# Performance work log

Measured on AMD Instinct MI355X. Metric: run time of the kernel, lower is better.

Reference implementation:

```python
import jax, jax.numpy as jnp
import numpy as np

N = 4096
D_IN = 512
D_H = 128
HEADS = 4
NEG_BIG = 1e10  # matches tf mask constant
LEAKY_ALPHA = 0.2  # tf.nn.leaky_relu default


def setup_inputs() -> dict:
    key = jax.random.key(0)
    ks = jax.random.split(key, 6)
    # 0/1 dense adjacency (faithful to tf.sparse.add producing dense 0/1 + mask)
    adjacency = jax.random.randint(ks[0], (N, N), 0, 2).astype(jnp.float32)
    # guarantee no empty rows (softmax over all -1e10 is degenerate)
    adjacency = adjacency.at[jnp.arange(N), jnp.arange(N)].set(1.0)
    input_feature = jax.random.normal(ks[1], (N, D_IN), dtype=jnp.float32)
    scale = 1.0 / np.sqrt(D_IN)
    kernels = jax.random.normal(ks[2], (HEADS, D_IN, D_H), dtype=jnp.float32) * scale
    biases = jnp.zeros((HEADS, D_H), dtype=jnp.float32)
    a_scale = 1.0 / np.sqrt(D_H)
    attn_self = jax.random.normal(ks[3], (HEADS, D_H), dtype=jnp.float32) * a_scale
    attn_neigh = jax.random.normal(ks[4], (HEADS, D_H), dtype=jnp.float32) * a_scale
    return {
        "adjacency": adjacency,
        "input_feature": input_feature,
        "kernels": kernels,
        "biases": biases,
        "attn_self": attn_self,
        "attn_neigh": attn_neigh,
    }


def reference(adjacency, input_feature, kernels, biases, attn_self, attn_neigh):
    # per-head feature projection: [H, N, D_h]
    feats = jnp.einsum("nd,hde->hne", input_feature, kernels)
    # additive attention logits
    a_s = jnp.einsum("hne,he->hn", feats, attn_self)   # [H, N]
    a_n = jnp.einsum("hne,he->hn", feats, attn_neigh)  # [H, N]
    dense = a_s[:, :, None] + a_n[:, None, :]          # [H, N, N]
    dense = jax.nn.leaky_relu(dense, negative_slope=LEAKY_ALPHA)
    mask = NEG_BIG * (adjacency - 1.0)                 # 0 where edge, -1e10 elsewhere
    dense = jax.nn.softmax(dense + mask[None, :, :], axis=-1)
    out = jnp.einsum("hnm,hme->hne", dense, feats) + biases[:, None, :]  # [H, N, D_h]
    # concat heads: [N, H*D_h]
    return jnp.transpose(out, (1, 0, 2)).reshape(out.shape[1], -1)
```

## Files before the change

### kernel.cpp

```cpp
#include <hip/hip_runtime.h>

#define NN 4096
#define DIN 512
#define DH 128
#define NH 4

typedef float f32x4 __attribute__((ext_vector_type(4)));
typedef _Float16 f16x8 __attribute__((ext_vector_type(8)));
typedef _Float16 f16x4 __attribute__((ext_vector_type(4)));

__device__ __forceinline__ float leaky(float x){ return x > 0.f ? x : 0.2f*x; }

__global__ __launch_bounds__(256) void k_pack(
    const float* __restrict__ adj, unsigned int* __restrict__ bmg)
{
  int tId = blockIdx.x*256 + threadIdx.x;
  const float* p = adj + (size_t)tId*32;
  unsigned int b = 0;
  #pragma unroll
  for (int k=0;k<8;k++){
    f32x4 v = *(const f32x4*)(p + k*4);
    #pragma unroll
    for (int q=0;q<4;q++) b |= (v[q] > 0.5f) ? (1u << (k*4+q)) : 0u;
  }
  bmg[tId] = b;
}

__global__ __launch_bounds__(256) void k_gemm1(
    const float* __restrict__ X, const float* __restrict__ Kw,
    const float* __restrict__ attn_s, const float* __restrict__ attn_n,
    _Float16* __restrict__ featsT, float* __restrict__ a_s, float* __restrict__ a_n)
{
  const int it = blockIdx.x, h = blockIdx.y;
  const int i0 = it*64;
  const int t = threadIdx.x, w = t>>6, lane = t&63;
  const int eoff = (w>>1)*64, ioff = (w&1)*32;
  const int lg = lane>>4, li = lane&15;

  __shared__ _Float16 KT[128][40];
  __shared__ _Float16 XT[64][40];
  __shared__ float red_s[2][2][2][16];
  __shared__ float red_n[2][2][2][16];

  f32x4 acc[4][2] = {};

  for (int ks=0; ks<16; ++ks){
    const int d0 = ks*32;
    __syncthreads();
    #pragma unroll
    for (int q=0;q<4;q++){
      int f = t + 256*q;
      int e = f & 127, dg = (f>>7)*4;
      f16x4 hv;
      #pragma unroll
      for (int k=0;k<4;k++)
        hv[k] = (_Float16)Kw[(h*DIN + d0 + dg + k)*DH + e];
      *(f16x4*)&KT[e][dg] = hv;
    }
    #pragma unroll
    for (int q=0;q<2;q++){
      int f = t + 256*q;
      int i = f>>3, s = (f&7)*4;
      f32x4 v = *(const f32x4*)&X[(i0+i)*DIN + d0 + s];
      f16x4 hv; hv[0]=(_Float16)v[0]; hv[1]=(_Float16)v[1];
      hv[2]=(_Float16)v[2]; hv[3]=(_Float16)v[3];
      *(f16x4*)&XT[i][s] = hv;
    }
    __syncthreads();
    f16x8 af[4], bf[2];
    #pragma unroll
    for (int ef=0; ef<4; ++ef) af[ef] = *(const f16x8*)&KT[eoff + ef*16 + li][lg*8];
    #pragma unroll
    for (int f2=0; f2<2; ++f2) bf[f2] = *(const f16x8*)&XT[ioff + f2*16 + li][lg*8];
    #pragma unroll
    for (int ef=0; ef<4; ++ef)
      #pragma unroll
      for (int f2=0; f2<2; ++f2)
        acc[ef][f2] = __builtin_amdgcn_mfma_f32_16x16x32_f16(af[ef], bf[f2], acc[ef][f2], 0,0,0);
  }

  float ps[2] = {0,0}, pn[2] = {0,0};
  #pragma unroll
  for (int ef=0; ef<4; ++ef){
    #pragma unroll
    for (int r=0;r<4;r++){
      int e = eoff + ef*16 + lg*4 + r;
      float as_e = attn_s[h*DH + e];
      float an_e = attn_n[h*DH + e];
      #pragma unroll
      for (int f2=0; f2<2; ++f2){
        int irow = i0 + ioff + f2*16 + li;
        float v = acc[ef][f2][r];
        featsT[(h*DH + e)*NN + irow] = (_Float16)v;
        ps[f2] += v*as_e; pn[f2] += v*an_e;
      }
    }
  }
  #pragma unroll
  for (int f2=0; f2<2; ++f2){
    ps[f2] += __shfl_xor(ps[f2], 16); ps[f2] += __shfl_xor(ps[f2], 32);
    pn[f2] += __shfl_xor(pn[f2], 16); pn[f2] += __shfl_xor(pn[f2], 32);
  }
  if (lane < 16){
    red_s[w>>1][w&1][0][lane] = ps[0]; red_s[w>>1][w&1][1][lane] = ps[1];
    red_n[w>>1][w&1][0][lane] = pn[0]; red_n[w>>1][w&1][1][lane] = pn[1];
  }
  __syncthreads();
  if (t < 64){
    int ih = t>>5, fb = (t>>4)&1, l2 = t&15;
    a_s[h*NN + i0 + t] = red_s[0][ih][fb][l2] + red_s[1][ih][fb][l2];
    a_n[h*NN + i0 + t] = red_n[0][ih][fb][l2] + red_n[1][ih][fb][l2];
  }
}

__global__ void k_amax(const float* __restrict__ a_n, float* __restrict__ Amax){
  int h = blockIdx.x, t = threadIdx.x;
  float m = -3.4e38f;
  for (int i=t; i<NN; i+=256) m = fmaxf(m, a_n[h*NN+i]);
  #pragma unroll
  for (int s=1; s<64; s<<=1) m = fmaxf(m, __shfl_xor(m, s));
  __shared__ float sm[4];
  if ((t&63)==0) sm[t>>6] = m;
  __syncthreads();
  if (t==0) Amax[h] = fmaxf(fmaxf(sm[0],sm[1]), fmaxf(sm[2],sm[3]));
}

__global__ __launch_bounds__(512, 4) void k_pv(
    const unsigned int* __restrict__ bmg, const _Float16* __restrict__ featsT,
    const float* __restrict__ a_s, const float* __restrict__ a_n,
    const float* __restrict__ Amax,
    _Float16* __restrict__ Opart, float* __restrict__ Dpart)
{
  const int it = blockIdx.x, h = blockIdx.y, jcI = blockIdx.z;
  const int i0 = it*128, j0 = jcI*1024;
  const int t = threadIdx.x, w = t>>6, lane = t&63;
  const int lg = lane>>4, li = lane&15;

  __shared__ _Float16 ft[128*32];
  __shared__ float an_s[1024];
  __shared__ unsigned char bm_s[128*144];

  if (t < 256) *(f32x4*)&an_s[t*4] = *(const f32x4*)&a_n[h*NN + j0 + t*4];
  #pragma unroll
  for (int p=0;p<2;p++){
    int rr = p*64 + (t>>3), c = t&7;
    uint4 v = *(const uint4*)((const char*)bmg + (size_t)(i0+rr)*(NN/8) + jcI*128 + c*16);
    *(uint4*)&bm_s[rr*144 + c*16] = v;
  }
  const int rowA = i0 + w*16 + li;
  const float asv = a_s[h*NN + rowA];
  const float mv = leaky(asv + Amax[h]);
  const float negmc = -mv * 1.44269504f;
  __syncthreads();

  f32x4 acc[8] = {};
  f32x4 accd = {};
  f16x8 ones;
  #pragma unroll
  for (int q=0;q<8;q++) ones[q] = (_Float16)1.0f;

  const int e_st = t>>2, c_st = t&3;
  const size_t src_row = (size_t)(h*DH + e_st)*NN + j0 + c_st*8;

  for (int js=0; js<32; ++js){
    __syncthreads();
    __builtin_amdgcn_global_load_lds(
        (const __attribute__((address_space(1))) void*)(featsT + src_row + js*32),
        (__attribute__((address_space(3))) void*)(&ft[t*8]),
        16, 0, 0);

    const int jb = js*32 + lg*8;
    f32x4 an0 = *(const f32x4*)&an_s[jb];
    f32x4 an1 = *(const f32x4*)&an_s[jb+4];
    unsigned int byte = bm_s[(w*16+li)*144 + js*4 + lg];
    f16x8 af;
    #pragma unroll
    for (int q=0;q<8;q++){
      float anv = (q<4) ? an0[q] : an1[q-4];
      float x = asv + anv;
      float l = fmaxf(x, 0.2f*x);
      float e2 = __builtin_exp2f(fmaf(l, 1.44269504f, negmc));
      float wv = (byte & (1u<<q)) ? e2 : 0.f;
      af[q] = (_Float16)wv;
    }
    __syncthreads();
    #pragma unroll
    for (int ef=0; ef<8; ++ef){
      f16x8 bfr = *(const f16x8*)&ft[(ef*16+li)*32 + lg*8];
      acc[ef] = __builtin_amdgcn_mfma_f32_16x16x32_f16(af, bfr, acc[ef], 0,0,0);
    }
    accd = __builtin_amdgcn_mfma_f32_16x16x32_f16(af, ones, accd, 0,0,0);
  }

  const size_t chb = (size_t)(jcI*4 + h)*NN;
  if (li == 0)
    *(f32x4*)&Dpart[chb + i0 + w*16 + lg*4] = accd;
  #pragma unroll
  for (int ef=0; ef<8; ++ef)
    #pragma unroll
    for (int r=0;r<4;r++){
      int row = i0 + w*16 + lg*4 + r;
      Opart[(chb + row)*DH + ef*16 + li] = (_Float16)acc[ef][r];
    }
}

__global__ __launch_bounds__(256) void k_out(
    const _Float16* __restrict__ Opart, const float* __restrict__ Dpart,
    const float* __restrict__ bias, float* __restrict__ out)
{
  int gid = blockIdx.x*256 + threadIdx.x;
  int base = gid*4;
  int i = base >> 9;
  int he = base & 511;
  int h = he >> 7;
  int e = he & 127;
  float n0=0,n1=0,n2=0,n3=0, den=0;
  #pragma unroll
  for (int jc=0; jc<4; ++jc){
    int ch = (jc*4+h)*NN + i;
    f16x4 v = *(const f16x4*)(Opart + (size_t)ch*DH + e);
    n0 += (float)v[0]; n1 += (float)v[1]; n2 += (float)v[2]; n3 += (float)v[3];
    den += Dpart[ch];
  }
  float inv = 1.f/den;
  f32x4 b4 = *(const f32x4*)&bias[he];
  f32x4 o; o[0]=n0*inv+b4[0]; o[1]=n1*inv+b4[1]; o[2]=n2*inv+b4[2]; o[3]=n3*inv+b4[3];
  *(f32x4*)&out[base] = o;
}

extern "C" void kernel_launch(void* const* d_in, const int* in_sizes, int n_in,
                              void* d_out, int out_size, void* d_ws, size_t ws_size,
                              hipStream_t stream)
{
  const float* adj   = (const float*)d_in[0];
  const float* X     = (const float*)d_in[1];
  const float* Kw    = (const float*)d_in[2];
  const float* bias  = (const float*)d_in[3];
  const float* atn_s = (const float*)d_in[4];
  const float* atn_n = (const float*)d_in[5];
  float* out = (float*)d_out;

  char* ws = (char*)d_ws;
  _Float16* featsT = (_Float16*)ws;
  unsigned int* bmg = (unsigned int*)(ws + ((size_t)4<<20));
  float* a_s  = (float*)(ws + (size_t)6*1024*1024);
  float* a_n  = a_s + NH*NN;
  float* Amax = a_n + NH*NN;
  float* Dpart = Amax + 64;
  _Float16* Opart = (_Float16*)(Dpart + 4*NH*NN);

  hipLaunchKernelGGL(k_pack, dim3(2048), dim3(256), 0, stream, adj, bmg);
  hipLaunchKernelGGL(k_gemm1, dim3(64,4), dim3(256), 0, stream,
                     X, Kw, atn_s, atn_n, featsT, a_s, a_n);
  hipLaunchKernelGGL(k_amax, dim3(4), dim3(256), 0, stream, a_n, Amax);
  hipLaunchKernelGGL(k_pv, dim3(32,4,4), dim3(512), 0, stream,
                     bmg, featsT, a_s, a_n, Amax, Opart, Dpart);
  hipLaunchKernelGGL(k_out, dim3(2048), dim3(256), 0, stream,
                     Opart, Dpart, bias, out);
}
```

Before: 85.36 us.

## Factor exp of leaky logits into per-row and per-column terms, double-buffer features

Uses the identity exp(leaky(as+an)-m) = max(E_i*ea_j, G_i*ga_j), with exp(an) and exp(0.2*an) computed once per column in the amax kernel, so the per-element exp in the attention-weight loop becomes two multiplies and a max. The PV kernel moves to 256 threads with each wave handling two 16-row tiles that share each B-fragment load. Feature tiles are double-buffered with async global-to-LDS loads and an XOR-swizzled layout, leaving one barrier per iteration. The trade-offs are more registers for the doubled accumulators, possible overflow or underflow of exp(an) in fp32, and extra global buffers for the precomputed exponentials.

```diff
diff --git a/kernel.cpp b/kernel.cpp
--- a/kernel.cpp
+++ b/kernel.cpp
@@ -4,6 +4,7 @@
 #define DIN 512
 #define DH 128
 #define NH 4
+#define L2E 1.44269504f
 
 typedef float f32x4 __attribute__((ext_vector_type(4)));
 typedef _Float16 f16x8 __attribute__((ext_vector_type(8)));
@@ -113,10 +114,16 @@
   }
 }
 
-__global__ void k_amax(const float* __restrict__ a_n, float* __restrict__ Amax){
+__global__ void k_amax(const float* __restrict__ a_n, float* __restrict__ Amax,
+                       float* __restrict__ EA_g, float* __restrict__ GA_g){
   int h = blockIdx.x, t = threadIdx.x;
   float m = -3.4e38f;
-  for (int i=t; i<NN; i+=256) m = fmaxf(m, a_n[h*NN+i]);
+  for (int i=t; i<NN; i+=256){
+    float v = a_n[h*NN+i];
+    m = fmaxf(m, v);
+    EA_g[h*NN+i] = __builtin_exp2f(v*L2E);
+    GA_g[h*NN+i] = __builtin_exp2f(0.2f*v*L2E);
+  }
   #pragma unroll
   for (int s=1; s<64; s<<=1) m = fmaxf(m, __shfl_xor(m, s));
   __shared__ float sm[4];
@@ -125,10 +132,10 @@
   if (t==0) Amax[h] = fmaxf(fmaxf(sm[0],sm[1]), fmaxf(sm[2],sm[3]));
 }
 
-__global__ __launch_bounds__(512, 4) void k_pv(
+__global__ __launch_bounds__(256, 3) void k_pv(
     const unsigned int* __restrict__ bmg, const _Float16* __restrict__ featsT,
-    const float* __restrict__ a_s, const float* __restrict__ a_n,
-    const float* __restrict__ Amax,
+    const float* __restrict__ a_s, const float* __restrict__ Amax,
+    const float* __restrict__ EA_g, const float* __restrict__ GA_g,
     _Float16* __restrict__ Opart, float* __restrict__ Dpart)
 {
   const int it = blockIdx.x, h = blockIdx.y, jcI = blockIdx.z;
@@ -136,71 +143,108 @@
   const int t = threadIdx.x, w = t>>6, lane = t&63;
   const int lg = lane>>4, li = lane&15;
 
-  __shared__ _Float16 ft[128*32];
-  __shared__ float an_s[1024];
+  __shared__ _Float16 ft[2][128*32];
+  __shared__ float EA_s[1024], GA_s[1024];
   __shared__ unsigned char bm_s[128*144];
 
-  if (t < 256) *(f32x4*)&an_s[t*4] = *(const f32x4*)&a_n[h*NN + j0 + t*4];
-  #pragma unroll
-  for (int p=0;p<2;p++){
-    int rr = p*64 + (t>>3), c = t&7;
-    uint4 v = *(const uint4*)((const char*)bmg + (size_t)(i0+rr)*(NN/8) + jcI*128 + c*16);
-    *(uint4*)&bm_s[rr*144 + c*16] = v;
-  }
-  const int rowA = i0 + w*16 + li;
-  const float asv = a_s[h*NN + rowA];
-  const float mv = leaky(asv + Amax[h]);
-  const float negmc = -mv * 1.44269504f;
+  __builtin_amdgcn_global_load_lds(
+      (const __attribute__((address_space(1))) void*)(EA_g + h*NN + j0 + t*4),
+      (__attribute__((address_space(3))) void*)(&EA_s[t*4]), 16, 0, 0);
+  __builtin_amdgcn_global_load_lds(
+      (const __attribute__((address_space(1))) void*)(GA_g + h*NN + j0 + t*4),
+      (__attribute__((address_space(3))) void*)(&GA_s[t*4]), 16, 0, 0);
+  #pragma unroll
+  for (int p=0;p<4;p++){
+    int idx = p*256 + t;
+    int r = idx>>3, c = idx&7;
+    uint4 v = *(const uint4*)((const char*)bmg + (size_t)(i0+r)*(NN/8) + jcI*128 + c*16);
+    *(uint4*)&bm_s[r*144 + c*16] = v;
+  }
+
+  const int r0 = w*32 + li, r1 = r0 + 16;
+  const float am = Amax[h];
+  const float as0 = a_s[h*NN + i0 + r0];
+  const float as1 = a_s[h*NN + i0 + r1];
+  const float m0 = leaky(as0 + am), m1 = leaky(as1 + am);
+  const float E0 = __builtin_exp2f((as0 - m0)*L2E);
+  const float G0 = __builtin_exp2f((0.2f*as0 - m0)*L2E);
+  const float E1 = __builtin_exp2f((as1 - m1)*L2E);
+  const float G1 = __builtin_exp2f((0.2f*as1 - m1)*L2E);
+
+  auto STAGE = [&](int buf, int js){
+    #pragma unroll
+    for (int q=0;q<2;q++){
+      int idx = q*256 + t;
+      int r = idx>>2, p = idx&3;
+      int l = p ^ ((r>>1)&3);
+      __builtin_amdgcn_global_load_lds(
+          (const __attribute__((address_space(1))) void*)(featsT + (size_t)(h*DH + r)*NN + j0 + js*32 + l*8),
+          (__attribute__((address_space(3))) void*)(&ft[buf][idx*8]), 16, 0, 0);
+    }
+  };
+
+  STAGE(0, 0);
   __syncthreads();
 
-  f32x4 acc[8] = {};
-  f32x4 accd = {};
+  f32x4 acc0[8] = {}, acc1[8] = {};
+  f32x4 accd0 = {}, accd1 = {};
   f16x8 ones;
   #pragma unroll
   for (int q=0;q<8;q++) ones[q] = (_Float16)1.0f;
 
-  const int e_st = t>>2, c_st = t&3;
-  const size_t src_row = (size_t)(h*DH + e_st)*NN + j0 + c_st*8;
+  const int slot = lg ^ ((li>>1)&3);
 
   for (int js=0; js<32; ++js){
+    const int cur = js&1;
+    if (js < 31) STAGE(cur^1, js+1);
+
+    const int jb = js*32 + lg*8;
+    f32x4 ea0 = *(const f32x4*)&EA_s[jb];
+    f32x4 ea1 = *(const f32x4*)&EA_s[jb+4];
+    f32x4 ga0 = *(const f32x4*)&GA_s[jb];
+    f32x4 ga1 = *(const f32x4*)&GA_s[jb+4];
+    unsigned int b0 = bm_s[r0*144 + js*4 + lg];
+    unsigned int b1 = bm_s[r1*144 + js*4 + lg];
+
+    f16x8 af0, af1;
+    #pragma unroll
+    for (int q=0;q<8;q++){
+      float ev = (q<4) ? ea0[q] : ea1[q-4];
+      float gv = (q<4) ? ga0[q] : ga1[q-4];
+      float w0 = fmaxf(E0*ev, G0*gv);
+      float w1 = fmaxf(E1*ev, G1*gv);
+      unsigned mq0 = (unsigned)(((int)(b0 << (31-q))) >> 31);
+      unsigned mq1 = (unsigned)(((int)(b1 << (31-q))) >> 31);
+      w0 = __builtin_bit_cast(float, __builtin_bit_cast(unsigned, w0) & mq0);
+      w1 = __builtin_bit_cast(float, __builtin_bit_cast(unsigned, w1) & mq1);
+      af0[q] = (_Float16)w0;
+      af1[q] = (_Float16)w1;
+    }
+
+    #pragma unroll
+    for (int ef=0; ef<8; ++ef){
+      f16x8 bfr = *(const f16x8*)&ft[cur][(ef*16+li)*32 + slot*8];
+      acc0[ef] = __builtin_amdgcn_mfma_f32_16x16x32_f16(af0, bfr, acc0[ef], 0,0,0);
+      acc1[ef] = __builtin_amdgcn_mfma_f32_16x16x32_f16(af1, bfr, acc1[ef], 0,0,0);
+    }
+    accd0 = __builtin_amdgcn_mfma_f32_16x16x32_f16(af0, ones, accd0, 0,0,0);
+    accd1 = __builtin_amdgcn_mfma_f32_16x16x32_f16(af1, ones, accd1, 0,0,0);
+
     __syncthreads();
-    __builtin_amdgcn_global_load_lds(
-        (const __attribute__((address_space(1))) void*)(featsT + src_row + js*32),
-        (__attribute__((address_space(3))) void*)(&ft[t*8]),
-        16, 0, 0);
-
-    const int jb = js*32 + lg*8;
-    f32x4 an0 = *(const f32x4*)&an_s[jb];
-    f32x4 an1 = *(const f32x4*)&an_s[jb+4];
-    unsigned int byte = bm_s[(w*16+li)*144 + js*4 + lg];
-    f16x8 af;
-    #pragma unroll
-    for (int q=0;q<8;q++){
-      float anv = (q<4) ? an0[q] : an1[q-4];
-      float x = asv + anv;
-      float l = fmaxf(x, 0.2f*x);
-      float e2 = __builtin_exp2f(fmaf(l, 1.44269504f, negmc));
-      float wv = (byte & (1u<<q)) ? e2 : 0.f;
-      af[q] = (_Float16)wv;
-    }
-    __syncthreads();
-    #pragma unroll
-    for (int ef=0; ef<8; ++ef){
-      f16x8 bfr = *(const f16x8*)&ft[(ef*16+li)*32 + lg*8];
-      acc[ef] = __builtin_amdgcn_mfma_f32_16x16x32_f16(af, bfr, acc[ef], 0,0,0);
-    }
-    accd = __builtin_amdgcn_mfma_f32_16x16x32_f16(af, ones, accd, 0,0,0);
   }
 
   const size_t chb = (size_t)(jcI*4 + h)*NN;
-  if (li == 0)
-    *(f32x4*)&Dpart[chb + i0 + w*16 + lg*4] = accd;
+  if (li == 0){
+    *(f32x4*)&Dpart[chb + i0 + w*32 + lg*4] = accd0;
+    *(f32x4*)&Dpart[chb + i0 + w*32 + 16 + lg*4] = accd1;
+  }
   #pragma unroll
   for (int ef=0; ef<8; ++ef)
     #pragma unroll
     for (int r=0;r<4;r++){
-      int row = i0 + w*16 + lg*4 + r;
-      Opart[(chb + row)*DH + ef*16 + li] = (_Float16)acc[ef][r];
+      int row0 = i0 + w*32 + lg*4 + r;
+      Opart[(chb + row0)*DH + ef*16 + li] = (_Float16)acc0[ef][r];
+      Opart[(chb + row0 + 16)*DH + ef*16 + li] = (_Float16)acc1[ef][r];
     }
 }
 
@@ -246,15 +290,17 @@
   float* a_s  = (float*)(ws + (size_t)6*1024*1024);
   float* a_n  = a_s + NH*NN;
   float* Amax = a_n + NH*NN;
-  float* Dpart = Amax + 64;
+  float* EA_g = Amax + 64;
+  float* GA_g = EA_g + NH*NN;
+  float* Dpart = GA_g + NH*NN;
   _Float16* Opart = (_Float16*)(Dpart + 4*NH*NN);
 
   hipLaunchKernelGGL(k_pack, dim3(2048), dim3(256), 0, stream, adj, bmg);
   hipLaunchKernelGGL(k_gemm1, dim3(64,4), dim3(256), 0, stream,
                      X, Kw, atn_s, atn_n, featsT, a_s, a_n);
-  hipLaunchKernelGGL(k_amax, dim3(4), dim3(256), 0, stream, a_n, Amax);
-  hipLaunchKernelGGL(k_pv, dim3(32,4,4), dim3(512), 0, stream,
-                     bmg, featsT, a_s, a_n, Amax, Opart, Dpart);
+  hipLaunchKernelGGL(k_amax, dim3(4), dim3(256), 0, stream, a_n, Amax, EA_g, GA_g);
+  hipLaunchKernelGGL(k_pv, dim3(32,4,4), dim3(256), 0, stream,
+                     bmg, featsT, a_s, Amax, EA_g, GA_g, Opart, Dpart);
   hipLaunchKernelGGL(k_out, dim3(2048), dim3(256), 0, stream,
                      Opart, Dpart, bias, out);
 }
```

Result: faster. 73.01 us (-14.5%).
